# Performance work log

Hardware: AMD Instinct MI355X
Metric: run time of the kernel (lower is better)

The kernel has to match this reference:

```python
import jax, jax.numpy as jnp
from jax import lax
import numpy as np

FRAME_LEN = 128
HOP = 64  # frame_len // 2 (default hop)
SAMPLE_LEN = 65536
IR_LEN = 1024

# torch.hann_window(N) is periodic: 0.5*(1 - cos(2*pi*n/N))
WIN = 0.5 * (1.0 - jnp.cos(2.0 * jnp.pi * jnp.arange(FRAME_LEN, dtype=jnp.float32) / FRAME_LEN))


def setup_inputs() -> dict:
    key = jax.random.key(0)
    k1, k2 = jax.random.split(key)
    x = jax.random.normal(k1, (1, SAMPLE_LEN), dtype=jnp.float32)
    IR = jax.random.normal(k2, (1, IR_LEN), dtype=jnp.float32)
    return {"x": x, "IR": IR}


def _scale_ir(ir2d):
    # get_MSG + scale_IR(target_gain = MSG + 2)
    spec = jnp.fft.rfft(ir2d[0])
    mag = jnp.abs(spec)
    phase = jnp.angle(spec)
    power = mag ** 2
    MLG = jnp.mean(power)
    zero_phase = (phase > -0.1) & (phase < 0.1)  # DC bin always qualifies
    peak_gain = jnp.max(jnp.where(zero_phase, power, -jnp.inf))
    MSG = -10.0 * jnp.log10(peak_gain / MLG)
    target_gain = MSG + 2.0
    mean_gain = 10.0 * jnp.log10(MLG)
    factor = jnp.power(jnp.float32(0.5), (target_gain - mean_gain) / 6.0)
    return ir2d / factor


def _howling(x1d, ir1d):
    L = x1d.shape[0]
    conv_len = FRAME_LEN + ir1d.shape[0] - 1
    # number of iterations that perform the feedback update (torch loop breaks
    # when frame_start + conv_len >= sample_len, AFTER adding to howling_out)
    n_fb = max(0, (L - conv_len - 1) // HOP)

    def step(x, i):
        fs = i * HOP
        frame = lax.dynamic_slice(x, (fs,), (FRAME_LEN,))
        w = WIN * frame
        conv = jnp.convolve(w, ir1d)  # mode='full', length conv_len
        fs2 = fs + HOP
        seg = lax.dynamic_slice(x, (fs2,), (conv_len,)) + conv
        x = lax.dynamic_update_slice(x, seg, (fs2,))
        x = jnp.clip(x, -1.0, 1.0)
        return x, w

    x_out, frames = lax.scan(step, x1d, jnp.arange(n_fb))
    # last iteration: windowed frame added to howling_out, then break (no feedback, no clamp)
    fs_last = n_fb * HOP
    last_w = WIN * lax.dynamic_slice(x_out, (fs_last,), (FRAME_LEN,))
    frames = jnp.concatenate([frames, last_w[None, :]], axis=0)  # [T, frame_len]
    T = n_fb + 1
    pos = (jnp.arange(T)[:, None] * HOP + jnp.arange(FRAME_LEN)[None, :]).reshape(-1)
    howl = jnp.zeros((L,), x1d.dtype).at[pos].add(frames.reshape(-1))
    return jnp.clip(howl, -1.0, 1.0)


def reference(x, IR):
    ir = _scale_ir(IR)
    out = _howling(x[0], ir[0])
    return out[None, :]
```

## Files before the change

### kernel.cpp

```cpp
#include <hip/hip_runtime.h>
#include <math.h>

#define FRAME 128
#define HOPW 64
#define SLEN 65536
#define IRLEN 1024
#define NFB 1006
#define RMASK 2047
#define PI_D 3.14159265358979323846

__device__ __forceinline__ float clip1(float v) { return fminf(1.0f, fmaxf(-1.0f, v)); }

__global__ __launch_bounds__(1024) void scale_ir_kernel(const float* __restrict__ ir,
                                                        float* __restrict__ irs) {
    __shared__ float xl[IRLEN];
    __shared__ float rmax[1024];
    __shared__ float rsum[1024];
    __shared__ float fbc;
    int tid = threadIdx.x;
    xl[tid] = ir[tid];
    __syncthreads();

    float pw = 0.f;
    int ok = 0;
    if (tid < 513) {
        double th = -2.0 * PI_D * (double)tid / 1024.0;
        double cr = cos(th), ci = sin(th);
        double wr = 1.0, wi = 0.0, re = 0.0, im = 0.0;
        for (int n = 0; n < IRLEN; ++n) {
            double xv = (double)xl[n];
            re += xv * wr;
            im += xv * wi;
            double nr = wr * cr - wi * ci;
            wi = wr * ci + wi * cr;
            wr = nr;
        }
        float mag = (float)sqrt(re * re + im * im);
        pw = mag * mag;
        double ph = atan2(im, re);
        ok = (ph > -0.1 && ph < 0.1) ? 1 : 0;
    }
    rmax[tid] = (tid < 513 && ok) ? pw : -INFINITY;
    rsum[tid] = (tid < 513) ? pw : 0.f;
    __syncthreads();
    for (int s = 512; s > 0; s >>= 1) {
        if (tid < s) {
            rmax[tid] = fmaxf(rmax[tid], rmax[tid + s]);
            rsum[tid] = rsum[tid] + rsum[tid + s];
        }
        __syncthreads();
    }
    if (tid == 0) {
        float peak = rmax[0];
        float MLG = rsum[0] / 513.0f;
        float MSG = -10.0f * log10f(peak / MLG);
        float target_gain = MSG + 2.0f;
        float mean_gain = 10.0f * log10f(MLG);
        fbc = powf(0.5f, (target_gain - mean_gain) / 6.0f);
    }
    __syncthreads();
    irs[tid] = ir[tid] / fbc;
}

__global__ __launch_bounds__(768) void howl_kernel(const float* __restrict__ x,
                                                   const float* __restrict__ irs,
                                                   float* __restrict__ out) {
    __shared__ float ring[2048];
    __shared__ float wlds[FRAME];
    __shared__ float winv[FRAME];
    __shared__ float tail[HOPW];
    __shared__ float part[4 * 1152];

    int tid = threadIdx.x;
    int lane = tid & 63;
    int kg = tid / 192;
    int ob = tid % 192;
    int q = ob * 6;
    int lo = q - kg * 32 - 31;

    float wir[37];
#pragma unroll
    for (int j = 0; j < 37; ++j) {
        int idx = lo + j;
        wir[j] = (idx >= 0 && idx < IRLEN) ? irs[idx] : 0.f;
    }

    if (tid < FRAME) winv[tid] = (float)(0.5 * (1.0 - cos(PI_D * (double)tid / 64.0)));
    if (tid < HOPW) tail[tid] = 0.f;
    for (int idx = tid; idx < 1216; idx += 768) ring[idx] = x[idx];
    __syncthreads();
    if (tid < FRAME) wlds[tid] = winv[tid] * ring[tid];
    __syncthreads();

#pragma unroll 1
    for (int i = 0; i < NFB; ++i) {
        int base = i * HOPW;

        float xv = 0.f;
        if (tid >= 64 && tid < 128) {
            int g = base + 1216 + (tid - 64);
            if (g < SLEN) xv = x[g];
        }
        float wreg = wlds[kg * 32 + (lane & 31)];
        float a0 = 0, a1 = 0, a2 = 0, a3 = 0, a4 = 0, a5 = 0;
#pragma unroll
        for (int kk = 0; kk < 32; ++kk) {
            float s = __int_as_float(__builtin_amdgcn_readlane(__float_as_int(wreg), 31 - kk));
            a0 = fmaf(s, wir[kk + 0], a0);
            a1 = fmaf(s, wir[kk + 1], a1);
            a2 = fmaf(s, wir[kk + 2], a2);
            a3 = fmaf(s, wir[kk + 3], a3);
            a4 = fmaf(s, wir[kk + 4], a4);
            a5 = fmaf(s, wir[kk + 5], a5);
        }
        if (tid < 64) {
            float w0 = wlds[tid];
            out[base + tid] = clip1(w0 + tail[tid]);
            tail[tid] = wlds[64 + tid];
        }
        float* pp = &part[kg * 1152 + q];
        pp[0] = a0; pp[1] = a1; pp[2] = a2; pp[3] = a3; pp[4] = a4; pp[5] = a5;
        __syncthreads();

        for (int p = tid; p < 1152; p += 768) {
            float s = part[p] + part[1152 + p] + part[2 * 1152 + p] + part[3 * 1152 + p];
            int slot = (base + 64 + p) & RMASK;
            float v = clip1(ring[slot] + s);
            ring[slot] = v;
            if (p < FRAME) wlds[p] = winv[p] * v;
        }
        if (tid >= 64 && tid < 128) {
            int slot = (base + 1216 + (tid - 64)) & RMASK;
            ring[slot] = clip1(xv);
        }
        __syncthreads();
    }

    if (tid < 64) out[64384 + tid] = clip1(wlds[tid] + tail[tid]);
    else if (tid < 128) out[64384 + tid] = clip1(wlds[tid]);
    for (int idx = 64512 + tid; idx < SLEN; idx += 768) out[idx] = 0.f;
}

extern "C" void kernel_launch(void* const* d_in, const int* in_sizes, int n_in,
                              void* d_out, int out_size, void* d_ws, size_t ws_size,
                              hipStream_t stream) {
    const float* x = (const float*)d_in[0];
    const float* ir = (const float*)d_in[1];
    float* out = (float*)d_out;
    float* irs = (float*)d_ws;

    hipLaunchKernelGGL(scale_ir_kernel, dim3(1), dim3(1024), 0, stream, ir, irs);
    hipLaunchKernelGGL(howl_kernel, dim3(1), dim3(768), 0, stream, x, irs, out);
}
```

Baseline: 1.213 ms.

## Fuse IR scaling into howling kernel and defer non-critical ring updates

Merges the IR-scaling kernel into the howling kernel so only one launch runs, and splits the DFT into four independent accumulator chains to shorten the dependency chain. Only the first 128 ring slots, which feed the next frame, are updated on the critical path. The remaining partial-sum reductions are double-buffered and applied during the next iteration alongside the convolution. It also prefetches the next x samples one iteration ahead and uses a lighter custom barrier. This shortens the serial per-iteration critical path at the cost of more shared memory and more delicate ordering reasoning.

Measured after the change: 1.058 ms. 12.8% less time.

```diff
diff --git a/kernel.cpp b/kernel.cpp
--- a/kernel.cpp
+++ b/kernel.cpp
@@ -11,97 +11,136 @@
 
 __device__ __forceinline__ float clip1(float v) { return fminf(1.0f, fmaxf(-1.0f, v)); }
 
-__global__ __launch_bounds__(1024) void scale_ir_kernel(const float* __restrict__ ir,
-                                                        float* __restrict__ irs) {
-    __shared__ float xl[IRLEN];
-    __shared__ float rmax[1024];
-    __shared__ float rsum[1024];
-    __shared__ float fbc;
-    int tid = threadIdx.x;
-    xl[tid] = ir[tid];
+__device__ __forceinline__ void loop_barrier() {
+    __builtin_amdgcn_sched_barrier(0);
+    asm volatile("s_waitcnt lgkmcnt(0)" ::: "memory");
+    __builtin_amdgcn_s_barrier();
+    __builtin_amdgcn_sched_barrier(0);
+}
+
+__global__ __launch_bounds__(768) void howl_fused(const float* __restrict__ x,
+                                                  const float* __restrict__ ir,
+                                                  float* __restrict__ out) {
+    __shared__ float ring[2048];
+    __shared__ float part[2][4][1152];
+    __shared__ float irl[IRLEN];
+    __shared__ float wlds[FRAME];
+    __shared__ float winv[FRAME];
+    __shared__ float tailb[HOPW];
+    __shared__ float red1[1024];
+    __shared__ float red2[1024];
+    __shared__ float invfs;
+
+    const int tid = threadIdx.x;
+    const int lane = tid & 63;
+    const int kg = tid / 192;
+    const int ob = tid % 192;
+    const int q = ob * 6;
+    const int lo = q - kg * 32 - 31;
+
+    for (int idx = tid; idx < IRLEN; idx += 768) irl[idx] = ir[idx];
+    for (int idx = tid; idx < 1216; idx += 768) ring[idx] = x[idx];
+    if (tid < FRAME) winv[tid] = (float)(0.5 * (1.0 - cos(PI_D * (double)tid / 64.0)));
+    if (tid < HOPW) tailb[tid] = 0.f;
+    if (tid >= 513) { red1[tid] = -INFINITY; red2[tid] = 0.f; }
+    if (tid < 256) { red1[768 + tid] = -INFINITY; red2[768 + tid] = 0.f; }
     __syncthreads();
 
-    float pw = 0.f;
-    int ok = 0;
     if (tid < 513) {
         double th = -2.0 * PI_D * (double)tid / 1024.0;
-        double cr = cos(th), ci = sin(th);
-        double wr = 1.0, wi = 0.0, re = 0.0, im = 0.0;
-        for (int n = 0; n < IRLEN; ++n) {
-            double xv = (double)xl[n];
-            re += xv * wr;
-            im += xv * wi;
-            double nr = wr * cr - wi * ci;
-            wi = wr * ci + wi * cr;
-            wr = nr;
+        double c4 = cos(4.0 * th), s4 = sin(4.0 * th);
+        double wr0 = 1.0,           wi0 = 0.0;
+        double wr1 = cos(th),       wi1 = sin(th);
+        double wr2 = cos(2.0 * th), wi2 = sin(2.0 * th);
+        double wr3 = cos(3.0 * th), wi3 = sin(3.0 * th);
+        double ar0 = 0, ai0 = 0, ar1 = 0, ai1 = 0, ar2 = 0, ai2 = 0, ar3 = 0, ai3 = 0;
+        for (int m = 0; m < 256; ++m) {
+            double x0 = irl[4 * m], x1 = irl[4 * m + 1], x2 = irl[4 * m + 2], x3 = irl[4 * m + 3];
+            ar0 += x0 * wr0; ai0 += x0 * wi0;
+            ar1 += x1 * wr1; ai1 += x1 * wi1;
+            ar2 += x2 * wr2; ai2 += x2 * wi2;
+            ar3 += x3 * wr3; ai3 += x3 * wi3;
+            double t;
+            t = wr0 * c4 - wi0 * s4; wi0 = wr0 * s4 + wi0 * c4; wr0 = t;
+            t = wr1 * c4 - wi1 * s4; wi1 = wr1 * s4 + wi1 * c4; wr1 = t;
+            t = wr2 * c4 - wi2 * s4; wi2 = wr2 * s4 + wi2 * c4; wr2 = t;
+            t = wr3 * c4 - wi3 * s4; wi3 = wr3 * s4 + wi3 * c4; wr3 = t;
         }
+        double re = (ar0 + ar1) + (ar2 + ar3);
+        double im = (ai0 + ai1) + (ai2 + ai3);
         float mag = (float)sqrt(re * re + im * im);
-        pw = mag * mag;
+        float pw = mag * mag;
         double ph = atan2(im, re);
-        ok = (ph > -0.1 && ph < 0.1) ? 1 : 0;
+        int ok = (ph > -0.1 && ph < 0.1) ? 1 : 0;
+        red1[tid] = ok ? pw : -INFINITY;
+        red2[tid] = pw;
     }
-    rmax[tid] = (tid < 513 && ok) ? pw : -INFINITY;
-    rsum[tid] = (tid < 513) ? pw : 0.f;
     __syncthreads();
     for (int s = 512; s > 0; s >>= 1) {
         if (tid < s) {
-            rmax[tid] = fmaxf(rmax[tid], rmax[tid + s]);
-            rsum[tid] = rsum[tid] + rsum[tid + s];
+            red1[tid] = fmaxf(red1[tid], red1[tid + s]);
+            red2[tid] = red2[tid] + red2[tid + s];
         }
         __syncthreads();
     }
     if (tid == 0) {
-        float peak = rmax[0];
-        float MLG = rsum[0] / 513.0f;
+        float peak = red1[0];
+        float MLG = red2[0] / 513.0f;
         float MSG = -10.0f * log10f(peak / MLG);
         float target_gain = MSG + 2.0f;
         float mean_gain = 10.0f * log10f(MLG);
-        fbc = powf(0.5f, (target_gain - mean_gain) / 6.0f);
+        invfs = powf(0.5f, (target_gain - mean_gain) / 6.0f);
     }
     __syncthreads();
-    irs[tid] = ir[tid] / fbc;
-}
 
-__global__ __launch_bounds__(768) void howl_kernel(const float* __restrict__ x,
-                                                   const float* __restrict__ irs,
-                                                   float* __restrict__ out) {
-    __shared__ float ring[2048];
-    __shared__ float wlds[FRAME];
-    __shared__ float winv[FRAME];
-    __shared__ float tail[HOPW];
-    __shared__ float part[4 * 1152];
-
-    int tid = threadIdx.x;
-    int lane = tid & 63;
-    int kg = tid / 192;
-    int ob = tid % 192;
-    int q = ob * 6;
-    int lo = q - kg * 32 - 31;
-
+    const float fbc = invfs;
     float wir[37];
 #pragma unroll
     for (int j = 0; j < 37; ++j) {
         int idx = lo + j;
-        wir[j] = (idx >= 0 && idx < IRLEN) ? irs[idx] : 0.f;
+        wir[j] = (idx >= 0 && idx < IRLEN) ? irl[idx] / fbc : 0.f;
     }
-
-    if (tid < FRAME) winv[tid] = (float)(0.5 * (1.0 - cos(PI_D * (double)tid / 64.0)));
-    if (tid < HOPW) tail[tid] = 0.f;
-    for (int idx = tid; idx < 1216; idx += 768) ring[idx] = x[idx];
-    __syncthreads();
+    float xv = 0.f;
+    if (tid >= 64 && tid < 128) xv = x[1216 + (tid - 64)];
     if (tid < FRAME) wlds[tid] = winv[tid] * ring[tid];
     __syncthreads();
 
+    int pb = 0;
 #pragma unroll 1
     for (int i = 0; i < NFB; ++i) {
-        int base = i * HOPW;
+        const int base = i * HOPW;
 
-        float xv = 0.f;
-        if (tid >= 64 && tid < 128) {
-            int g = base + 1216 + (tid - 64);
-            if (g < SLEN) xv = x[g];
+        float wreg = wlds[kg * 32 + (lane & 31)];
+
+        if (tid < 64) {
+            float w0 = wlds[tid];
+            float w1 = wlds[64 + tid];
+            out[base + tid] = clip1(w0 + tailb[tid]);
+            tailb[tid] = w1;
+        } else if (tid < 128) {
+            int t = tid - 64;
+            int pos = base + 1216 + t;
+            if (pos < SLEN) ring[pos & RMASK] = clip1(xv);
+            int npos = pos + HOPW;
+            xv = (npos < SLEN) ? x[npos] : 0.f;
         }
-        float wreg = wlds[kg * 32 + (lane & 31)];
+
+        if (i > 0) {
+            const float* pprev = &part[pb ^ 1][0][0];
+            {
+                int p = 128 + tid;
+                int slot = (base + p) & RMASK;
+                float s = pprev[p] + pprev[1152 + p] + pprev[2 * 1152 + p] + pprev[3 * 1152 + p];
+                ring[slot] = clip1(ring[slot] + s);
+            }
+            if (tid >= 256 && tid < 512) {
+                int p = 896 + (tid - 256);
+                int slot = (base + p) & RMASK;
+                float s = pprev[p] + pprev[1152 + p] + pprev[2 * 1152 + p] + pprev[3 * 1152 + p];
+                ring[slot] = clip1(ring[slot] + s);
+            }
+        }
+
         float a0 = 0, a1 = 0, a2 = 0, a3 = 0, a4 = 0, a5 = 0;
 #pragma unroll
         for (int kk = 0; kk < 32; ++kk) {
@@ -113,30 +152,27 @@
             a4 = fmaf(s, wir[kk + 4], a4);
             a5 = fmaf(s, wir[kk + 5], a5);
         }
-        if (tid < 64) {
-            float w0 = wlds[tid];
-            out[base + tid] = clip1(w0 + tail[tid]);
-            tail[tid] = wlds[64 + tid];
-        }
-        float* pp = &part[kg * 1152 + q];
-        pp[0] = a0; pp[1] = a1; pp[2] = a2; pp[3] = a3; pp[4] = a4; pp[5] = a5;
-        __syncthreads();
+        float* pp = &part[pb][kg][q];
+        *(float2*)(pp + 0) = make_float2(a0, a1);
+        *(float2*)(pp + 2) = make_float2(a2, a3);
+        *(float2*)(pp + 4) = make_float2(a4, a5);
 
-        for (int p = tid; p < 1152; p += 768) {
-            float s = part[p] + part[1152 + p] + part[2 * 1152 + p] + part[3 * 1152 + p];
-            int slot = (base + 64 + p) & RMASK;
+        loop_barrier();
+
+        if (tid < 128) {
+            const float* pcur = &part[pb][0][0];
+            int slot = (base + 64 + tid) & RMASK;
+            float s = pcur[tid] + pcur[1152 + tid] + pcur[2 * 1152 + tid] + pcur[3 * 1152 + tid];
             float v = clip1(ring[slot] + s);
             ring[slot] = v;
-            if (p < FRAME) wlds[p] = winv[p] * v;
+            wlds[tid] = winv[tid] * v;
         }
-        if (tid >= 64 && tid < 128) {
-            int slot = (base + 1216 + (tid - 64)) & RMASK;
-            ring[slot] = clip1(xv);
-        }
-        __syncthreads();
+
+        loop_barrier();
+        pb ^= 1;
     }
 
-    if (tid < 64) out[64384 + tid] = clip1(wlds[tid] + tail[tid]);
+    if (tid < 64) out[64384 + tid] = clip1(wlds[tid] + tailb[tid]);
     else if (tid < 128) out[64384 + tid] = clip1(wlds[tid]);
     for (int idx = 64512 + tid; idx < SLEN; idx += 768) out[idx] = 0.f;
 }
@@ -147,8 +183,7 @@
     const float* x = (const float*)d_in[0];
     const float* ir = (const float*)d_in[1];
     float* out = (float*)d_out;
-    float* irs = (float*)d_ws;
+    (void)d_ws; (void)ws_size; (void)in_sizes; (void)n_in; (void)out_size;
 
-    hipLaunchKernelGGL(scale_ir_kernel, dim3(1), dim3(1024), 0, stream, ir, irs);
-    hipLaunchKernelGGL(howl_kernel, dim3(1), dim3(768), 0, stream, x, irs, out);
+    hipLaunchKernelGGL(howl_fused, dim3(1), dim3(768), 0, stream, x, ir, out);
 }
```
